# Optimization experiments

Measured on AMD Instinct MI355X. Metric: run time of the kernel, lower is better.

The kernel has to match this reference:

```python
import jax, jax.numpy as jnp
import numpy as np

D_MODEL = 192
D_STATE = 16
D_CONV = 4
EXPAND = 2
HEADDIM = 16
D_INNER = EXPAND * D_MODEL          # 384
NHEADS = D_INNER // HEADDIM         # 24
NGROUPS = 1
CHUNK = 256
BATCH = 2
SEQLEN = 8192
D_IN_PROJ = 2 * D_INNER + NGROUPS * D_STATE + NHEADS   # 808
D_IN_PROJ_B = NGROUPS * D_STATE                         # 16
CONV_DIM = D_INNER + NGROUPS * D_STATE                  # 400
EPS = 1e-5


def silu(x):
    return x * jax.nn.sigmoid(x)


def causal_dwconv(x, w, b):
    # x: (B, L, C), w: (C, 1, K) depthwise, b: (C,). Causal: left-pad K-1.
    C = x.shape[-1]
    xt = jnp.transpose(x, (0, 2, 1))  # (B, C, L)
    y = jax.lax.conv_general_dilated(
        xt, w, window_strides=(1,), padding=[(D_CONV - 1, 0)],
        dimension_numbers=('NCH', 'OIH', 'NCH'), feature_group_count=C)
    return jnp.transpose(y + b[None, :, None], (0, 2, 1))


def segsum(x):
    # x: (..., T) -> (..., T, T) lower-triangular segment sums (exclusive of j, inclusive of i)
    T = x.shape[-1]
    cs = jnp.cumsum(x, axis=-1)
    seg = cs[..., :, None] - cs[..., None, :]
    mask = jnp.tril(jnp.ones((T, T), dtype=bool))
    return jnp.where(mask, seg, -jnp.inf)


def ssd(x, dt, A, Bm, Cm):
    # Mamba2 chunked selective scan (mamba_chunk_scan_combined semantics).
    # x:(b,l,h,p) dt:(b,l,h) A:(h,) Bm,Cm:(b,l,g,n)
    b, l, h, p = x.shape
    g = Bm.shape[2]
    Bm = jnp.repeat(Bm, h // g, axis=2)  # (b,l,h,n)
    Cm = jnp.repeat(Cm, h // g, axis=2)
    nchunks = l // CHUNK
    tochunk = lambda t: t.reshape(b, nchunks, CHUNK, *t.shape[2:])
    xc, dtc, Bc, Cc = map(tochunk, (x, dt, Bm, Cm))
    a = jnp.transpose(dtc * A, (0, 3, 1, 2))        # (b,h,c,cl)
    a_cum = jnp.cumsum(a, axis=-1)                   # (b,h,c,cl)
    Lmat = jnp.exp(segsum(a))                        # (b,h,c,cl,cl)
    xdt = xc * dtc[..., None]                        # (b,c,cl,h,p)
    # intra-chunk (diagonal) output
    Y_diag = jnp.einsum('bclhn,bcshn,bhcls,bcshp->bclhp', Cc, Bc, Lmat, xdt)
    # per-chunk end states
    decay_states = jnp.exp(a_cum[..., -1:] - a_cum)  # (b,h,c,cl)
    states = jnp.einsum('bclhn,bhcl,bclhp->bchpn', Bc, decay_states, xdt)
    # inter-chunk recurrence (associative, via chunk-level segsum)
    init = jnp.zeros_like(states[:, :1])
    states = jnp.concatenate([init, states], axis=1)              # (b,c+1,h,p,n)
    a_chunk = jnp.pad(a_cum[..., -1], ((0, 0), (0, 0), (1, 0)))   # (b,h,c+1)
    decay_chunk = jnp.exp(segsum(a_chunk))                        # (b,h,c+1,c+1)
    states = jnp.einsum('bhzc,bchpn->bzhpn', decay_chunk, states)[:, :-1]  # (b,c,h,p,n)
    # state -> output within each chunk
    Y_off = jnp.einsum('bclhn,bchpn,bhcl->bclhp', Cc, states, jnp.exp(a_cum))
    return (Y_diag + Y_off).reshape(b, l, h, p)


def setup_inputs() -> dict:
    key = jax.random.key(0)
    ks = jax.random.split(key, 12)
    rng = np.random.default_rng(0)
    u = jax.random.normal(ks[0], (BATCH, SEQLEN, D_MODEL), dtype=jnp.float32)
    support = jax.random.normal(ks[1], (BATCH, SEQLEN, D_MODEL), dtype=jnp.float32)
    W_in = jax.random.normal(ks[2], (D_IN_PROJ, D_MODEL), dtype=jnp.float32) * 0.02
    W_in_b = jax.random.normal(ks[3], (D_IN_PROJ_B, D_MODEL), dtype=jnp.float32) * 0.02
    conv_w = jax.random.normal(ks[4], (CONV_DIM, 1, D_CONV), dtype=jnp.float32) * 0.2
    conv_b = jnp.zeros((CONV_DIM,), dtype=jnp.float32)
    conv_w_b = jax.random.normal(ks[5], (D_IN_PROJ_B, 1, D_CONV), dtype=jnp.float32) * 0.2
    conv_b_b = jnp.zeros((D_IN_PROJ_B,), dtype=jnp.float32)
    # dt_bias init per the module (inverse-softplus of dt in [1e-3, 1e-1])
    dt = np.exp(rng.uniform(size=(NHEADS,)) * (np.log(0.1) - np.log(0.001)) + np.log(0.001))
    dt = np.clip(dt, 1e-4, None)
    dt_bias = jnp.asarray(dt + np.log(-np.expm1(-dt)), dtype=jnp.float32)
    A_log = jnp.asarray(np.log(rng.uniform(1.0, 16.0, size=(NHEADS,))), dtype=jnp.float32)
    D = jnp.ones((NHEADS,), dtype=jnp.float32)
    norm_w = jnp.ones((D_INNER,), dtype=jnp.float32)
    W_out = jax.random.normal(ks[6], (D_MODEL, D_INNER), dtype=jnp.float32) * 0.02
    return {'u': u, 'support': support, 'W_in': W_in, 'W_in_b': W_in_b,
            'conv_w': conv_w, 'conv_b': conv_b, 'conv_w_b': conv_w_b, 'conv_b_b': conv_b_b,
            'dt_bias': dt_bias, 'A_log': A_log, 'D': D, 'norm_w': norm_w, 'W_out': W_out}


def reference(u, support, W_in, W_in_b, conv_w, conv_b, conv_w_b, conv_b_b,
              dt_bias, A_log, D, norm_w, W_out):
    bsz, l, _ = u.shape
    zxbdt = u @ W_in.T                                  # (b,l,808)
    c = support @ W_in_b.T                              # (b,l,16)
    z = zxbdt[..., :D_INNER]
    xB = zxbdt[..., D_INNER:D_INNER + CONV_DIM]
    dt = jax.nn.softplus(zxbdt[..., -NHEADS:] + dt_bias)  # (b,l,h)
    A = -jnp.exp(A_log)
    xB = silu(causal_dwconv(xB, conv_w, conv_b))
    Cv = silu(causal_dwconv(c, conv_w_b, conv_b_b))
    x = xB[..., :D_INNER]
    Bv = xB[..., D_INNER:]
    xh = x.reshape(bsz, l, NHEADS, HEADDIM)
    Bg = Bv.reshape(bsz, l, NGROUPS, D_STATE)
    Cg = Cv.reshape(bsz, l, NGROUPS, D_STATE)
    y = ssd(xh, dt, A, Bg, Cg) + D[None, None, :, None] * xh
    y = y.reshape(bsz, l, D_INNER)
    # RMSNormGated, norm_before_gate=False: normalize(y * silu(z)) * weight
    yg = y * silu(z)
    yn = yg * jax.lax.rsqrt(jnp.mean(yg * yg, axis=-1, keepdims=True) + EPS) * norm_w
    return yn @ W_out.T
```

## Files before the change

kernel.cpp:

```cpp
#include <hip/hip_runtime.h>
#include <cmath>

#define ROWS      16384
#define SEQLEN    8192
#define BATCH     2
#define NHEADS    24
#define HEADDIM   16
#define D_STATE   16
#define D_INNER   384
#define D_MODEL   192
#define D_IN_PROJ 808
#define CONV_DIM  400
#define NCHUNKS   32
#define CHUNK     256
#define EPS       1e-5f
#define LOG2E     1.44269504088896f

typedef short bf16x8 __attribute__((ext_vector_type(8)));
typedef short bf16x4 __attribute__((ext_vector_type(4)));
typedef float f32x4  __attribute__((ext_vector_type(4)));
typedef unsigned short us4v __attribute__((ext_vector_type(4)));
typedef unsigned short us8v __attribute__((ext_vector_type(8)));
typedef unsigned int  u32x4 __attribute__((ext_vector_type(4)));

#if __has_builtin(__builtin_amdgcn_mfma_f32_16x16x16bf16_1k)
#define MFMA16(a, b, c) __builtin_amdgcn_mfma_f32_16x16x16bf16_1k((a), (b), (c), 0, 0, 0)
#define HAVE_MFMA16 1
#elif __has_builtin(__builtin_amdgcn_mfma_f32_16x16x16_bf16)
#define MFMA16(a, b, c) __builtin_amdgcn_mfma_f32_16x16x16_bf16((a), (b), (c), 0, 0, 0)
#define HAVE_MFMA16 1
#else
#define HAVE_MFMA16 0
#endif

__device__ __forceinline__ float silu_f(float x) { return x / (1.0f + expf(-x)); }
__device__ __forceinline__ float softplus_f(float x) { return (x > 20.0f) ? x : log1pf(expf(x)); }
__device__ __forceinline__ unsigned short f2bf(float x) {
  unsigned u = __builtin_bit_cast(unsigned, x);
  u += 0x7fff + ((u >> 16) & 1);
  return (unsigned short)(u >> 16);
}
__device__ __forceinline__ float bf2f(unsigned short s) {
  unsigned u = (unsigned)s << 16;
  return __builtin_bit_cast(float, u);
}
__device__ __forceinline__ unsigned pk_bf(float a, float b) {
  unsigned ua = __builtin_bit_cast(unsigned, a) + 0x7fffu;
  unsigned ub = __builtin_bit_cast(unsigned, b) + 0x7fffu;
  return __builtin_amdgcn_perm(ub, ua, 0x07060302u);
}

__global__ __launch_bounds__(256)
void cvt3_kernel(const float* __restrict__ a, unsigned short* __restrict__ ao, long na,
                 const float* __restrict__ b, unsigned short* __restrict__ bo, long nb,
                 const float* __restrict__ c, unsigned short* __restrict__ co, long nc) {
  const long t0 = na >> 2, t1 = t0 + (nb >> 2), t2 = t1 + (nc >> 2);
  const long stride = (long)gridDim.x * blockDim.x;
  for (long i = (long)blockIdx.x * blockDim.x + threadIdx.x; i < t2; i += stride) {
    const float4* s; us4v* d; long j;
    if (i < t0)      { s = (const float4*)a; d = (us4v*)ao; j = i; }
    else if (i < t1) { s = (const float4*)b; d = (us4v*)bo; j = i - t0; }
    else             { s = (const float4*)c; d = (us4v*)co; j = i - t1; }
    float4 v = s[j];
    us4v o = { f2bf(v.x), f2bf(v.y), f2bf(v.z), f2bf(v.w) };
    d[j] = o;
  }
}

template<bool A_F32, bool OUT_BF16, bool ROUTE>
__launch_bounds__(256, 3)
__global__ void gemm_bf16(const void* __restrict__ Ap,
                          const unsigned short* __restrict__ W,
                          void* __restrict__ Cp, int M, int N, int K,
                          unsigned short* __restrict__ zbuf,
                          unsigned short* __restrict__ xT,
                          unsigned short* __restrict__ Braw,
                          unsigned short* __restrict__ draw) {
  constexpr int BM = 128, BN = 128, BK = 32, LDK = 40;
  __shared__ unsigned short As[2][BM * LDK];
  __shared__ unsigned short Ws[2][BN * LDK];
  const int tid  = threadIdx.x;
  const int wid  = tid >> 6, lane = tid & 63;
  const int wr   = wid >> 1, wc = wid & 1;
  const int fr   = lane & 15, fq = lane >> 4;
  const long m0  = (long)blockIdx.y * BM;
  const int  n0  = blockIdx.x * BN;

  f32x4 acc[4][4] = {};

  auto stage = [&](int k0, int buf) {
    if (A_F32) {
      const float* A = (const float*)Ap;
#pragma unroll
      for (int p = 0; p < 2; ++p) {
        int flat = p * 2048 + tid * 8;
        int r = flat >> 5, c = flat & 31;
        const float4* src = (const float4*)(A + (m0 + r) * (long)K + k0 + c);
        float4 v0 = src[0], v1 = src[1];
        us8v o = { f2bf(v0.x), f2bf(v0.y), f2bf(v0.z), f2bf(v0.w),
                   f2bf(v1.x), f2bf(v1.y), f2bf(v1.z), f2bf(v1.w) };
        *(us8v*)&As[buf][r * LDK + c] = o;
      }
    } else {
      const unsigned short* A = (const unsigned short*)Ap;
#pragma unroll
      for (int p = 0; p < 2; ++p) {
        int flat = p * 2048 + tid * 8;
        int r = flat >> 5, c = flat & 31;
        us8v v = *(const us8v*)(A + (m0 + r) * (long)K + k0 + c);
        *(us8v*)&As[buf][r * LDK + c] = v;
      }
    }
#pragma unroll
    for (int p = 0; p < 2; ++p) {
      int flat = p * 2048 + tid * 8;
      int r = flat >> 5, c = flat & 31;
      int gn = n0 + r;
      us8v v = { 0, 0, 0, 0, 0, 0, 0, 0 };
      if (gn < N) v = *(const us8v*)(W + (long)gn * K + k0 + c);
      *(us8v*)&Ws[buf][r * LDK + c] = v;
    }
  };

  const int nk = K / BK;
  stage(0, 0);
  __syncthreads();
  for (int kt = 0; kt < nk; ++kt) {
    const int cur = kt & 1;
    if (kt + 1 < nk) stage((kt + 1) * BK, cur ^ 1);
    bf16x8 af[4], bfr[4];
#pragma unroll
    for (int m = 0; m < 4; ++m)
      af[m] = *(const bf16x8*)&As[cur][(wr * 64 + m * 16 + fr) * LDK + fq * 8];
#pragma unroll
    for (int n = 0; n < 4; ++n)
      bfr[n] = *(const bf16x8*)&Ws[cur][(wc * 64 + n * 16 + fr) * LDK + fq * 8];
#pragma unroll
    for (int m = 0; m < 4; ++m)
#pragma unroll
      for (int n = 0; n < 4; ++n)
        acc[m][n] = __builtin_amdgcn_mfma_f32_16x16x32_bf16(bfr[n], af[m], acc[m][n], 0, 0, 0);
    __syncthreads();
  }

#pragma unroll
  for (int m = 0; m < 4; ++m) {
    const long gm = m0 + wr * 64 + m * 16 + fr;
#pragma unroll
    for (int n = 0; n < 4; ++n) {
      const int gn = n0 + wc * 64 + n * 16 + fq * 4;
      if (gn < N) {
        if (ROUTE) {
          us4v o = { f2bf(acc[m][n][0]), f2bf(acc[m][n][1]),
                     f2bf(acc[m][n][2]), f2bf(acc[m][n][3]) };
          const int bb = (int)(gm >> 13);
          const long t = gm & 8191;
          if (gn < 384) {
            *(us4v*)(zbuf + gm * 384 + gn) = o;
          } else if (gn < 768) {
            const int c = gn - 384, hh = c >> 4, ii = c & 15;
            *(us4v*)(xT + (((size_t)(bb * NHEADS + hh) * SEQLEN + t) << 4) + ii) = o;
          } else if (gn < 784) {
            *(us4v*)(Braw + gm * 16 + (gn - 768)) = o;
          } else {
            *(us4v*)(draw + gm * 24 + (gn - 784)) = o;
          }
        } else if (OUT_BF16) {
          us4v o = { f2bf(acc[m][n][0]), f2bf(acc[m][n][1]),
                     f2bf(acc[m][n][2]), f2bf(acc[m][n][3]) };
          *(us4v*)((unsigned short*)Cp + gm * N + gn) = o;
        } else {
          float4 o = make_float4(acc[m][n][0], acc[m][n][1], acc[m][n][2], acc[m][n][3]);
          *(float4*)((float*)Cp + gm * N + gn) = o;
        }
      }
    }
  }
}

#define CBC_NB  (ROWS * 4 / 256)
#define CDT_NB  (ROWS * 3 / 256)

__global__ __launch_bounds__(256)
void conv_bcdt(const unsigned short* __restrict__ Braw, const unsigned short* __restrict__ craw,
               const unsigned short* __restrict__ draw,
               const float* __restrict__ conv_w, const float* __restrict__ conv_b,
               const float* __restrict__ conv_w_b, const float* __restrict__ conv_b_b,
               const float* __restrict__ dt_bias,
               unsigned short* __restrict__ Bo, unsigned short* __restrict__ Co,
               float* __restrict__ dtoT) {
  const int blk = blockIdx.x;
  const us8v z8 = { 0, 0, 0, 0, 0, 0, 0, 0 };

  if (blk < CBC_NB) {
    const int idx = blk * 256 + threadIdx.x;
    const int row = idx / 4, q = idx % 4;
    const int b = row / SEQLEN, t = row % SEQLEN;

    const unsigned short* src = (q < 2) ? Braw : craw;
    const float* cw = (q < 2) ? conv_w + 384 * 4 : conv_w_b;
    const float* cb = (q < 2) ? conv_b + 384 : conv_b_b;
    const int c0 = (q & 1) * 8;
    const unsigned short* base = src + (size_t)row * D_STATE + c0;
    us8v x0 = (t >= 3) ? *(const us8v*)(base - 3 * D_STATE) : z8;
    us8v x1 = (t >= 2) ? *(const us8v*)(base - 2 * D_STATE) : z8;
    us8v x2 = (t >= 1) ? *(const us8v*)(base - 1 * D_STATE) : z8;
    us8v x3 = *(const us8v*)base;
    us8v o;
#pragma unroll
    for (int ch = 0; ch < 8; ++ch) {
      const float4 wv = *(const float4*)(cw + (c0 + ch) * 4);
      float acc = cb[c0 + ch] + wv.x * bf2f(x0[ch]) + wv.y * bf2f(x1[ch])
                + wv.z * bf2f(x2[ch]) + wv.w * bf2f(x3[ch]);
      o[ch] = f2bf(silu_f(acc));
    }
    if (q < 2) *(us8v*)(Bo + (size_t)row * D_STATE + c0) = o;
    else       *(us8v*)(Co + (size_t)row * D_STATE + c0) = o;
  } else {
    const int idx = (blk - CBC_NB) * 256 + threadIdx.x;
    const int row = idx / 3, q = idx % 3;
    const int b = row / SEQLEN, t = row % SEQLEN;
    const int h0 = q * 8;
    us8v dv = *(const us8v*)(draw + (size_t)row * 24 + h0);
#pragma unroll
    for (int j = 0; j < 8; ++j) {
      float v = bf2f(dv[j]) + dt_bias[h0 + j];
      dtoT[(size_t)(b * NHEADS + h0 + j) * SEQLEN + t] = softplus_f(v);
    }
  }
}

__global__ __launch_bounds__(512, 4)
void ssd_mfma_kernel(const unsigned short* __restrict__ xT, const unsigned short* __restrict__ Bo,
                     const unsigned short* __restrict__ Co, const float* __restrict__ dtoT,
                     const float* __restrict__ A_log, const float* __restrict__ conv_w,
                     const float* __restrict__ conv_b, const float* __restrict__ Dvec,
                     unsigned short* __restrict__ YdT, float* __restrict__ acum_g,
                     float* __restrict__ csum_g, float* __restrict__ stloc) {
  const int h    = blockIdx.x;
  const int cidx = blockIdx.y;
  const int b    = blockIdx.z;
  const int tid  = threadIdx.x;
  const int wid  = tid >> 6, lane = tid & 63;
  const int fr   = lane & 15, g = lane >> 4;

  __shared__ unsigned short Bs[256 * 24 + 32];
  __shared__ unsigned short xsT[16 * 264];
  __shared__ unsigned short BwT[16 * 264];
  __shared__ unsigned short xraw[259 * 16 + 8];
  __shared__ float sc2[CHUNK];
  __shared__ float scE[16];
  __shared__ float wsum[4];

  const float Ah = -expf(A_log[h]);
  const us8v z8 = { 0, 0, 0, 0, 0, 0, 0, 0 };

  float v = 0.f;
  if (tid < CHUNK) {
    v = dtoT[(size_t)(b * NHEADS + h) * SEQLEN + (size_t)cidx * CHUNK + tid] * Ah;
#pragma unroll
    for (int off = 1; off < 64; off <<= 1) {
      float u = __shfl_up(v, off, 64);
      if (lane >= off) v += u;
    }
    if (lane == 63) wsum[wid] = v;
  }

  const int r  = tid >> 1;
  const int hf = tid & 1;
  const size_t rowbase = (size_t)b * SEQLEN + (size_t)cidx * CHUNK;
  const size_t rhrow = (size_t)(b * NHEADS + h) * SEQLEN + (size_t)cidx * CHUNK + r;
  const float rdtv = dtoT[rhrow];
  us8v bh = ((const us8v*)(Bo + (rowbase + r) * D_STATE))[hf];
  if (hf == 0) *(us8v*)&Bs[r * 24 + 16] = z8;
  if (tid < 32) Bs[256 * 24 + tid] = 0;
  {
    const int tg = cidx * CHUNK + r - 3;
    us8v xv = z8;
    if (tg >= 0)
      xv = *(const us8v*)(xT + (((size_t)(b * NHEADS + h) * SEQLEN + tg) << 4) + 8 * hf);
    *(us8v*)&xraw[r * 16 + 8 * hf] = xv;
    if (tid < 6) {
      const int rr2 = 256 + (tid >> 1);
      const int hf2 = tid & 1;
      const int tg2 = cidx * CHUNK + rr2 - 3;
      us8v xv2 = *(const us8v*)(xT + (((size_t)(b * NHEADS + h) * SEQLEN + tg2) << 4) + 8 * hf2);
      *(us8v*)&xraw[rr2 * 16 + 8 * hf2] = xv2;
    }
  }
  __syncthreads();

  us8v xsil, xdt8;
  {
    us8v tA = *(const us8v*)&xraw[(r + 0) * 16 + 8 * hf];
    us8v tB = *(const us8v*)&xraw[(r + 1) * 16 + 8 * hf];
    us8v tC = *(const us8v*)&xraw[(r + 2) * 16 + 8 * hf];
    us8v tD = *(const us8v*)&xraw[(r + 3) * 16 + 8 * hf];
    const int cbase = h * HEADDIM + 8 * hf;
#pragma unroll
    for (int ch = 0; ch < 8; ++ch) {
      const float4 wv = *(const float4*)(conv_w + (cbase + ch) * 4);
      float acc = conv_b[cbase + ch] + wv.x * bf2f(tA[ch]) + wv.y * bf2f(tB[ch])
                + wv.z * bf2f(tC[ch]) + wv.w * bf2f(tD[ch]);
      float sv = silu_f(acc);
      xsil[ch] = f2bf(sv);
      xdt8[ch] = f2bf(sv * rdtv);
    }
  }
  const float ctot  = wsum[0] + wsum[1] + wsum[2] + wsum[3];
  const float ctot2 = ctot * LOG2E;
  if (tid < CHUNK) {
    float pre = 0.f;
#pragma unroll
    for (int w = 0; w < 4; ++w) if (w < wid) pre += wsum[w];
    v += pre;
    sc2[tid] = v * LOG2E;
    acum_g[(size_t)(b * NHEADS + h) * SEQLEN + (size_t)cidx * CHUNK + tid] = v;
    if (tid == CHUNK - 1) csum_g[(b * NHEADS + h) * NCHUNKS + cidx] = v;
  }
  __syncthreads();

  *(us8v*)&xraw[(r + 3) * 16 + 8 * hf] = xsil;
#pragma unroll
  for (int q = 0; q < 8; ++q)
    xsT[(q + 8 * hf) * 264 + r] = xdt8[q];
  {
    const float wdv = exp2f(ctot2 - sc2[r]);
    const float ed  = exp2f(sc2[r | 15] - sc2[r]);
    us8v bscaled;
#pragma unroll
    for (int q = 0; q < 8; ++q) {
      BwT[(q + 8 * hf) * 264 + r] = f2bf(bf2f(bh[q]) * wdv);
      bscaled[q] = f2bf(bf2f(bh[q]) * ed);
    }
    *(us8v*)&Bs[r * 24 + 8 * hf] = bscaled;
  }
  if (tid < 16) scE[tid] = sc2[tid * 16 + 15];
  __syncthreads();

  if (wid == 0) {
    f32x4 accS = {};
#pragma unroll
    for (int k2 = 0; k2 < 8; ++k2) {
      bf16x8 af = *(const bf16x8*)&BwT[fr * 264 + 32 * k2 + 8 * g];
      bf16x8 bb = *(const bf16x8*)&xsT[fr * 264 + 32 * k2 + 8 * g];
      accS = __builtin_amdgcn_mfma_f32_16x16x32_bf16(af, bb, accS, 0, 0, 0);
    }
    *(f32x4*)&stloc[((size_t)(b * NCHUNKS + cidx) * NHEADS + h) * 256 + fr * 16 + 4 * g] = accS;
  }

  const f32x4 zf = { 0.f, 0.f, 0.f, 0.f };
  const unsigned short* Cbase = Co + rowbase * D_STATE;
  const float Dh = Dvec[h];
  const int strips[2] = { wid, 15 - wid };

  bf16x8 brawq[2];
#pragma unroll
  for (int q = 0; q < 2; ++q) {
    us8v bv = z8;
    if (g < 2)
      bv = *(const us8v*)(Bo + (rowbase + strips[q] * 16 + fr) * D_STATE + 8 * g);
    brawq[q] = __builtin_bit_cast(bf16x8, bv);
  }

#if HAVE_MFMA16
#pragma unroll
  for (int q = 0; q < 2; ++q) {
    const int lt = strips[q];
    f32x4 acc = zf;
    bf16x8 cf = { 0, 0, 0, 0, 0, 0, 0, 0 };
    if (g < 2) cf = *(const bf16x8*)(Cbase + (size_t)(lt * 16 + fr) * D_STATE + 8 * g);
    const float acl2 = sc2[lt * 16 + fr];
    const int   lg   = lt * 16 + fr;
    for (int st = 0; st <= lt; ++st) {
      uint2 pp;
      if (st < lt) {
        bf16x8 bfg = *(const bf16x8*)&Bs[(st * 16 + fr) * 24 + 8 * g];
        f32x4 G = __builtin_amdgcn_mfma_f32_16x16x32_bf16(bfg, cf, zf, 0, 0, 0);
        const float wl = exp2f(acl2 - scE[st]);
        pp.x = pk_bf(G[0] * wl, G[1] * wl);
        pp.y = pk_bf(G[2] * wl, G[3] * wl);
      } else {
        f32x4 G = __builtin_amdgcn_mfma_f32_16x16x32_bf16(brawq[q], cf, zf, 0, 0, 0);
        f32x4 se2 = *(const f32x4*)&sc2[st * 16 + 4 * g];
        const int sbase = st * 16 + 4 * g;
        float w0 = (sbase + 0 <= lg) ? exp2f(acl2 - se2[0]) : 0.f;
        float w1 = (sbase + 1 <= lg) ? exp2f(acl2 - se2[1]) : 0.f;
        float w2 = (sbase + 2 <= lg) ? exp2f(acl2 - se2[2]) : 0.f;
        float w3 = (sbase + 3 <= lg) ? exp2f(acl2 - se2[3]) : 0.f;
        pp.x = pk_bf(G[0] * w0, G[1] * w1);
        pp.y = pk_bf(G[2] * w2, G[3] * w3);
      }
      const bf16x4 p4 = __builtin_bit_cast(bf16x4, pp);
      const bf16x4 x4 = *(const bf16x4*)&xsT[fr * 264 + st * 16 + 4 * g];
      acc = MFMA16(x4, p4, acc);
    }
    us4v xs4 = *(const us4v*)&xraw[(lt * 16 + fr + 3) * 16 + 4 * g];
    us4v o = { f2bf(acc[0] + Dh * bf2f(xs4[0])),
               f2bf(acc[1] + Dh * bf2f(xs4[1])),
               f2bf(acc[2] + Dh * bf2f(xs4[2])),
               f2bf(acc[3] + Dh * bf2f(xs4[3])) };
    *(us4v*)(YdT + (rhrow - r + (size_t)lt * 16 + fr) * HEADDIM + 4 * g) = o;
  }
#else
  const int Ls0 = fr + ((g & 1) << 5);
  const int Ls1 = Ls0 + 16;
  const bool hiq = (g >= 2);
#pragma unroll
  for (int q = 0; q < 2; ++q) {
    const int lt = strips[q];
    f32x4 acc = zf;
    bf16x8 cf = { 0, 0, 0, 0, 0, 0, 0, 0 };
    if (g < 2) cf = *(const bf16x8*)(Cbase + (size_t)(lt * 16 + fr) * D_STATE + 8 * g);
    const float acl2 = sc2[lt * 16 + fr];
    const int   lg   = lt * 16 + fr;
    const int npair = (lt + 2) >> 1;
    for (int sp = 0; sp < npair; ++sp) {
      uint2 pk[2];
#pragma unroll
      for (int ti = 0; ti < 2; ++ti) {
        const int st = 2 * sp + ti;
        if (st < lt) {
          bf16x8 bfg = *(const bf16x8*)&Bs[(st * 16 + fr) * 24 + 8 * g];
          f32x4 G = __builtin_amdgcn_mfma_f32_16x16x32_bf16(bfg, cf, zf, 0, 0, 0);
          const float wl = exp2f(acl2 - scE[st]);
          pk[ti].x = pk_bf(G[0] * wl, G[1] * wl);
          pk[ti].y = pk_bf(G[2] * wl, G[3] * wl);
        } else if (st == lt) {
          f32x4 G = __builtin_amdgcn_mfma_f32_16x16x32_bf16(brawq[q], cf, zf, 0, 0, 0);
          f32x4 se2 = *(const f32x4*)&sc2[st * 16 + 4 * g];
          const int sbase = st * 16 + 4 * g;
          float w0 = (sbase + 0 <= lg) ? exp2f(acl2 - se2[0]) : 0.f;
          float w1 = (sbase + 1 <= lg) ? exp2f(acl2 - se2[1]) : 0.f;
          float w2 = (sbase + 2 <= lg) ? exp2f(acl2 - se2[2]) : 0.f;
          float w3 = (sbase + 3 <= lg) ? exp2f(acl2 - se2[3]) : 0.f;
          pk[ti].x = pk_bf(G[0] * w0, G[1] * w1);
          pk[ti].y = pk_bf(G[2] * w2, G[3] * w3);
        } else {
          pk[ti].x = 0u; pk[ti].y = 0u;
        }
      }
      const int a00 = __shfl((int)pk[0].x, Ls0, 64);
      const int a10 = __shfl((int)pk[0].y, Ls0, 64);
      const int a01 = __shfl((int)pk[0].x, Ls1, 64);
      const int a11 = __shfl((int)pk[0].y, Ls1, 64);
      const int b00 = __shfl((int)pk[1].x, Ls0, 64);
      const int b10 = __shfl((int)pk[1].y, Ls0, 64);
      const int b01 = __shfl((int)pk[1].x, Ls1, 64);
      const int b11 = __shfl((int)pk[1].y, Ls1, 64);
      u32x4 pw;
      pw[0] = (unsigned)(hiq ? b00 : a00);
      pw[1] = (unsigned)(hiq ? b10 : a10);
      pw[2] = (unsigned)(hiq ? b01 : a01);
      pw[3] = (unsigned)(hiq ? b11 : a11);
      const bf16x8 pf = __builtin_bit_cast(bf16x8, pw);
      const bf16x8 xf = *(const bf16x8*)&xsT[fr * 264 + sp * 32 + 8 * g];
      acc = __builtin_amdgcn_mfma_f32_16x16x32_bf16(xf, pf, acc, 0, 0, 0);
    }
    us4v xs4 = *(const us4v*)&xraw[(lt * 16 + fr + 3) * 16 + 4 * g];
    us4v o = { f2bf(acc[0] + Dh * bf2f(xs4[0])),
               f2bf(acc[1] + Dh * bf2f(xs4[1])),
               f2bf(acc[2] + Dh * bf2f(xs4[2])),
               f2bf(acc[3] + Dh * bf2f(xs4[3])) };
    *(us4v*)(YdT + (rhrow - r + (size_t)lt * 16 + fr) * HEADDIM + 4 * g) = o;
  }
#endif
}

__global__ __launch_bounds__(256)
void chunk_scan_kernel(const float* __restrict__ stloc, const float* __restrict__ csum_g,
                       float* __restrict__ stpre) {
  const int b  = blockIdx.x / NHEADS;
  const int h  = blockIdx.x % NHEADS;
  const int pn = threadIdx.x;
  float S = 0.0f;
  for (int c = 0; c < NCHUNKS; ++c) {
    const size_t idx = ((size_t)(b * NCHUNKS + c) * NHEADS + h) * 256 + pn;
    stpre[idx] = S;
    S = __expf(csum_g[(b * NHEADS + h) * NCHUNKS + c]) * S + stloc[idx];
  }
}

#define TT 16
__global__ __launch_bounds__(384)
void yoff_norm_tiled(const unsigned short* __restrict__ YdT,
                     const unsigned short* __restrict__ Co, const float* __restrict__ acum_g,
                     const float* __restrict__ stpre,
                     const unsigned short* __restrict__ zbuf, const float* __restrict__ norm_w,
                     unsigned short* __restrict__ yn) {
  const int r0   = blockIdx.x * TT;
  const int b    = r0 / SEQLEN;
  const int t0   = r0 % SEQLEN;
  const int cidx = t0 / CHUNK;
  const int d    = threadIdx.x;
  const int h    = d >> 4, p = d & 15;
  const int wv   = d >> 6;

  __shared__ unsigned short Yt[NHEADS * TT * 16];
  __shared__ float At[NHEADS * TT];
  __shared__ float Ct[TT * 16];
  __shared__ float red[TT][6];

  {
    us8v* Yt8 = (us8v*)Yt;
#pragma unroll
    for (int rep = 0; rep < 2; ++rep) {
      int j = d + rep * 384;
      int hh = j >> 5, q = j & 31;
      const size_t src = ((size_t)(b * NHEADS + hh) * SEQLEN + t0) * HEADDIM + q * 8;
      Yt8[j] = *(const us8v*)(YdT + src);
    }
    At[d] = acum_g[(size_t)(b * NHEADS + (d >> 4)) * SEQLEN + t0 + (d & 15)];
    if (d < TT * 16) Ct[d] = bf2f(Co[(size_t)r0 * D_STATE + d]);
  }

  float S[16];
  {
    const float* Sp = stpre + ((size_t)(b * NCHUNKS + cidx) * NHEADS + h) * 256 + p * 16;
#pragma unroll
    for (int q = 0; q < 4; ++q) {
      float4 v4 = *(const float4*)(Sp + 4 * q);
      S[4 * q + 0] = v4.x; S[4 * q + 1] = v4.y; S[4 * q + 2] = v4.z; S[4 * q + 3] = v4.w;
    }
  }
  const float nw = norm_w[d];
  __syncthreads();

  float yg[TT];
#pragma unroll
  for (int tt = 0; tt < TT; ++tt) {
    float dot = 0.f;
#pragma unroll
    for (int n = 0; n < 16; ++n) dot += Ct[tt * 16 + n] * S[n];
    const float acl = At[h * TT + tt];
    float y = bf2f(Yt[h * 256 + tt * 16 + p]) + __expf(acl) * dot;
    const float z = bf2f(zbuf[(size_t)(r0 + tt) * 384 + d]);
    yg[tt] = y * silu_f(z);
    float s = yg[tt] * yg[tt];
#pragma unroll
    for (int off = 32; off > 0; off >>= 1) s += __shfl_down(s, off);
    if ((d & 63) == 0) red[tt][wv] = s;
  }
  __syncthreads();

#pragma unroll
  for (int tt = 0; tt < TT; ++tt) {
    const float tot = red[tt][0] + red[tt][1] + red[tt][2] + red[tt][3] + red[tt][4] + red[tt][5];
    const float scale = rsqrtf(tot * (1.0f / D_INNER) + EPS);
    yn[(size_t)(r0 + tt) * D_INNER + d] = f2bf(yg[tt] * scale * nw);
  }
}

extern "C" void kernel_launch(void* const* d_in, const int* in_sizes, int n_in,
                              void* d_out, int out_size, void* d_ws, size_t ws_size,
                              hipStream_t stream) {
  const float* u        = (const float*)d_in[0];
  const float* support  = (const float*)d_in[1];
  const float* W_in     = (const float*)d_in[2];
  const float* W_in_b   = (const float*)d_in[3];
  const float* conv_w   = (const float*)d_in[4];
  const float* conv_b   = (const float*)d_in[5];
  const float* conv_w_b = (const float*)d_in[6];
  const float* conv_b_b = (const float*)d_in[7];
  const float* dt_bias  = (const float*)d_in[8];
  const float* A_log    = (const float*)d_in[9];
  const float* Dvec     = (const float*)d_in[10];
  const float* norm_w   = (const float*)d_in[11];
  const float* W_out    = (const float*)d_in[12];
  float* out = (float*)d_out;
  char* wsb  = (char*)d_ws;

  unsigned short* Wi_b  = (unsigned short*)(wsb);
  unsigned short* Wo_b  = Wi_b + (size_t)D_IN_PROJ * D_MODEL;
  unsigned short* Wib_b = Wo_b + (size_t)D_MODEL * D_INNER;
  unsigned short* zbuf  = Wib_b + (size_t)D_STATE * D_MODEL;
  unsigned short* xT    = zbuf + (size_t)ROWS * D_INNER;
  unsigned short* Braw  = xT + (size_t)ROWS * D_INNER;
  unsigned short* draw  = Braw + (size_t)ROWS * D_STATE;
  unsigned short* craw  = draw + (size_t)ROWS * NHEADS;
  unsigned short* Bo    = craw + (size_t)ROWS * D_STATE;
  unsigned short* Co    = Bo + (size_t)ROWS * D_STATE;
  unsigned short* YdT   = Co + (size_t)ROWS * D_STATE;
  unsigned short* yn    = YdT + (size_t)ROWS * D_INNER;
  float* dtoT  = (float*)(yn + (size_t)ROWS * D_INNER);
  float* acum  = dtoT  + (size_t)ROWS * NHEADS;
  float* csum  = acum  + (size_t)BATCH * NHEADS * SEQLEN;
  float* stloc = csum  + (size_t)BATCH * NHEADS * NCHUNKS;
  float* stpre = stloc + (size_t)BATCH * NCHUNKS * NHEADS * 256;

  cvt3_kernel<<<224, 256, 0, stream>>>(W_in, Wi_b, (long)D_IN_PROJ * D_MODEL,
                                       W_out, Wo_b, (long)D_MODEL * D_INNER,
                                       W_in_b, Wib_b, (long)D_STATE * D_MODEL);
  gemm_bf16<true, true, true><<<dim3(7, ROWS / 128), 256, 0, stream>>>(
      u, Wi_b, nullptr, ROWS, D_IN_PROJ, D_MODEL, zbuf, xT, Braw, draw);
  gemm_bf16<true, true, false><<<dim3(1, ROWS / 128), 256, 0, stream>>>(
      support, Wib_b, craw, ROWS, D_STATE, D_MODEL, nullptr, nullptr, nullptr, nullptr);
  conv_bcdt<<<CBC_NB + CDT_NB, 256, 0, stream>>>(
      Braw, craw, draw, conv_w, conv_b, conv_w_b, conv_b_b, dt_bias, Bo, Co, dtoT);
  ssd_mfma_kernel<<<dim3(NHEADS, NCHUNKS, BATCH), 512, 0, stream>>>(
      xT, Bo, Co, dtoT, A_log, conv_w, conv_b, Dvec, YdT, acum, csum, stloc);
  chunk_scan_kernel<<<BATCH * NHEADS, 256, 0, stream>>>(stloc, csum, stpre);
  yoff_norm_tiled<<<ROWS / TT, 384, 0, stream>>>(YdT, Co, acum, stpre, zbuf, norm_w, yn);
  gemm_bf16<false, false, false><<<dim3((D_MODEL + 127) / 128, ROWS / 128), 256, 0, stream>>>(
      yn, Wo_b, out, ROWS, D_MODEL, D_INNER, nullptr, nullptr, nullptr, nullptr);
}
```

Before: 124.1 us.

## Fuse output projection GEMM into gated RMSNorm kernel via MFMA

The normalized bf16 activations are kept in shared memory, and each block runs the output-projection GEMM itself with MFMA instructions, writing the fp32 output directly. This removes the global write and re-read of the intermediate yn buffer and drops one kernel launch. In exchange, each 16-row block re-reads the whole W_out matrix from global memory or cache, and the GEMM tile is small (16 rows) with no LDS staging of the weights. The block's shared-memory footprint also grows.

```diff
diff --git a/kernel.cpp b/kernel.cpp
--- a/kernel.cpp
+++ b/kernel.cpp
@@ -482,12 +482,14 @@
 }
 
 #define TT 16
+#define LDY 392
 __global__ __launch_bounds__(384)
-void yoff_norm_tiled(const unsigned short* __restrict__ YdT,
-                     const unsigned short* __restrict__ Co, const float* __restrict__ acum_g,
-                     const float* __restrict__ stpre,
-                     const unsigned short* __restrict__ zbuf, const float* __restrict__ norm_w,
-                     unsigned short* __restrict__ yn) {
+void yoff_norm_gemm(const unsigned short* __restrict__ YdT,
+                    const unsigned short* __restrict__ Co, const float* __restrict__ acum_g,
+                    const float* __restrict__ stpre,
+                    const unsigned short* __restrict__ zbuf, const float* __restrict__ norm_w,
+                    const unsigned short* __restrict__ Wo,
+                    float* __restrict__ out) {
   const int r0   = blockIdx.x * TT;
   const int b    = r0 / SEQLEN;
   const int t0   = r0 % SEQLEN;
@@ -497,6 +499,7 @@
   const int wv   = d >> 6;
 
   __shared__ unsigned short Yt[NHEADS * TT * 16];
+  __shared__ unsigned short ynL[TT * LDY];
   __shared__ float At[NHEADS * TT];
   __shared__ float Ct[TT * 16];
   __shared__ float red[TT][6];
@@ -547,7 +550,28 @@
   for (int tt = 0; tt < TT; ++tt) {
     const float tot = red[tt][0] + red[tt][1] + red[tt][2] + red[tt][3] + red[tt][4] + red[tt][5];
     const float scale = rsqrtf(tot * (1.0f / D_INNER) + EPS);
-    yn[(size_t)(r0 + tt) * D_INNER + d] = f2bf(yg[tt] * scale * nw);
+    ynL[tt * LDY + d] = f2bf(yg[tt] * scale * nw);
+  }
+  __syncthreads();
+
+  const int lane = d & 63;
+  const int fr = lane & 15, fq = lane >> 4;
+  const int n0 = wv * 32;
+  f32x4 accg[2] = {};
+#pragma unroll
+  for (int kt = 0; kt < 12; ++kt) {
+    const bf16x8 af = *(const bf16x8*)&ynL[fr * LDY + kt * 32 + 8 * fq];
+#pragma unroll
+    for (int ct = 0; ct < 2; ++ct) {
+      const int col = n0 + ct * 16 + fr;
+      const bf16x8 bfr = *(const bf16x8*)(Wo + (size_t)col * D_INNER + kt * 32 + 8 * fq);
+      accg[ct] = __builtin_amdgcn_mfma_f32_16x16x32_bf16(bfr, af, accg[ct], 0, 0, 0);
+    }
+  }
+#pragma unroll
+  for (int ct = 0; ct < 2; ++ct) {
+    float4 o = make_float4(accg[ct][0], accg[ct][1], accg[ct][2], accg[ct][3]);
+    *(float4*)(out + (size_t)(r0 + fr) * D_MODEL + n0 + ct * 16 + fq * 4) = o;
   }
 }
 
@@ -581,8 +605,7 @@
   unsigned short* Bo    = craw + (size_t)ROWS * D_STATE;
   unsigned short* Co    = Bo + (size_t)ROWS * D_STATE;
   unsigned short* YdT   = Co + (size_t)ROWS * D_STATE;
-  unsigned short* yn    = YdT + (size_t)ROWS * D_INNER;
-  float* dtoT  = (float*)(yn + (size_t)ROWS * D_INNER);
+  float* dtoT  = (float*)(YdT + (size_t)ROWS * D_INNER);
   float* acum  = dtoT  + (size_t)ROWS * NHEADS;
   float* csum  = acum  + (size_t)BATCH * NHEADS * SEQLEN;
   float* stloc = csum  + (size_t)BATCH * NHEADS * NCHUNKS;
@@ -600,7 +623,6 @@
   ssd_mfma_kernel<<<dim3(NHEADS, NCHUNKS, BATCH), 512, 0, stream>>>(
       xT, Bo, Co, dtoT, A_log, conv_w, conv_b, Dvec, YdT, acum, csum, stloc);
   chunk_scan_kernel<<<BATCH * NHEADS, 256, 0, stream>>>(stloc, csum, stpre);
-  yoff_norm_tiled<<<ROWS / TT, 384, 0, stream>>>(YdT, Co, acum, stpre, zbuf, norm_w, yn);
-  gemm_bf16<false, false, false><<<dim3((D_MODEL + 127) / 128, ROWS / 128), 256, 0, stream>>>(
-      yn, Wo_b, out, ROWS, D_MODEL, D_INNER, nullptr, nullptr, nullptr, nullptr);
-}
+  yoff_norm_gemm<<<ROWS / TT, 384, 0, stream>>>(YdT, Co, acum, stpre, zbuf, norm_w,
+                                                Wo_b, out);
+}
```

Result: faster. 120.9 us (-2.6%).
